# Performance work log

Hardware: AMD Instinct MI355X
Metric: run time of the kernel (lower is better)

Reference implementation:

```python
import jax, jax.numpy as jnp
import numpy as np

BN_EPS = 1e-5
L2_EPS = 1e-12


def setup_inputs() -> dict:
    key = jax.random.key(0)
    k1, k2, k3 = jax.random.split(key, 3)
    B, N, D, K, G = 32, 2048, 512, 64, 16
    init_sc = 1.0 / np.sqrt(D)
    x = jax.random.normal(k1, (B, N, D), dtype=jnp.float32)
    clusters = init_sc * jax.random.normal(k2, (D, K + G), dtype=jnp.float32)
    clusters2 = init_sc * jax.random.normal(k3, (1, D, K), dtype=jnp.float32)
    bn_gamma = jnp.ones((K + G,), dtype=jnp.float32)
    bn_beta = jnp.zeros((K + G,), dtype=jnp.float32)
    return {"x": x, "clusters": clusters, "clusters2": clusters2,
            "bn_gamma": bn_gamma, "bn_beta": bn_beta}


def reference(x, clusters, clusters2, bn_gamma, bn_beta):
    B, N, D = x.shape
    K = clusters2.shape[-1]
    xf = x.reshape(B * N, D)
    # soft cluster assignment: [B*N, K+G]
    assn = xf @ clusters
    # BatchNorm1d (training-mode batch statistics, biased variance)
    mean = jnp.mean(assn, axis=0)
    var = jnp.var(assn, axis=0)
    assn = (assn - mean) * jax.lax.rsqrt(var + BN_EPS) * bn_gamma + bn_beta
    # softmax over clusters, then drop ghost clusters
    assn = jax.nn.softmax(assn, axis=1)[:, :K].reshape(B, N, K)
    # residual aggregation
    a_sum = jnp.sum(assn, axis=1, keepdims=True)          # [B, 1, K]
    a = a_sum * clusters2                                  # [B, D, K]
    vlad = jnp.einsum("bnk,bnd->bdk", assn, x) - a         # [B, D, K]
    # intra-normalization across feature dim D
    vlad = vlad / jnp.maximum(jnp.linalg.norm(vlad, axis=1, keepdims=True), L2_EPS)
    # flatten and global L2 normalization
    vlad = vlad.reshape(B, D * K)
    vlad = vlad / jnp.maximum(jnp.linalg.norm(vlad, axis=1, keepdims=True), L2_EPS)
    return vlad
```

## Files before the change

kernel.cpp:

```cpp
#include <hip/hip_runtime.h>
#include <hip/hip_bf16.h>
#include <stdint.h>

typedef __attribute__((ext_vector_type(8))) short short8;
typedef __attribute__((ext_vector_type(4))) float f32x4;

__device__ __forceinline__ float b2f(uint16_t u) {
  union { uint32_t i; float f; } v; v.i = ((uint32_t)u) << 16; return v.f;
}
__device__ __forceinline__ uint16_t f2b(float f) {
  uint32_t u = __float_as_uint(f);
  return (uint16_t)((u + 0x7FFFu + ((u >> 16) & 1u)) >> 16);
}
__device__ __forceinline__ uint32_t pk2(uint32_t lo, uint32_t hi) {
  return __builtin_amdgcn_perm(hi + 0x8000u, lo + 0x8000u, 0x07060302u);
}

__global__ void k0_prep(const float* __restrict__ clusters,
                        uint16_t* __restrict__ cB) {
  int gid = blockIdx.x * 256 + threadIdx.x;
  if (gid < 40960) {
    int i = gid & 7, chunk = gid >> 3;
    int lr = chunk & 15, q = (chunk >> 4) & 3, c5 = chunk >> 6;
    int n = c5 % 5, kk = c5 / 5;
    cB[gid] = f2b(clusters[(kk * 32 + q * 8 + i) * 80 + n * 16 + lr]);
  }
}

__global__ __launch_bounds__(256, 4) void k1_gemm1(
    const float* __restrict__ x, const uint16_t* __restrict__ cB,
    float* __restrict__ raw, float* __restrict__ part) {
  __shared__ float sf[1280];
  const int t = threadIdx.x;
  const int w = t >> 6, lane = t & 63, q = lane >> 4, lr = lane & 15;
  const int rbase = blockIdx.x * 64 + w * 16;

  f32x4 acc[5];
#pragma unroll
  for (int n = 0; n < 5; ++n) acc[n] = 0.f;

  const float* xa = x + (size_t)(rbase + lr) * 512 + q * 8;
  const short8* cbq = (const short8*)cB + q * 16 + lr;

  uint4 u0[2], u1[2];
  u0[0] = *(const uint4*)(xa);          u1[0] = *(const uint4*)(xa + 4);
  u0[1] = *(const uint4*)(xa + 32);     u1[1] = *(const uint4*)(xa + 36);
  short8 bfc[5], bfp[5];
#pragma unroll
  for (int n = 0; n < 5; ++n) bfc[n] = cbq[n * 64];

#pragma unroll
  for (int kk = 0; kk < 16; ++kk) {
    const int si = kk & 1;
    union { short8 s; uint32_t u[4]; } av;
    av.u[0] = pk2(u0[si].x, u0[si].y); av.u[1] = pk2(u0[si].z, u0[si].w);
    av.u[2] = pk2(u1[si].x, u1[si].y); av.u[3] = pk2(u1[si].z, u1[si].w);
    if (kk < 15) {
#pragma unroll
      for (int n = 0; n < 5; ++n) bfp[n] = cbq[((kk + 1) * 5 + n) * 64];
    }
    if (kk < 14) {
      u0[si] = *(const uint4*)(xa + (kk + 2) * 32);
      u1[si] = *(const uint4*)(xa + (kk + 2) * 32 + 4);
    }
#pragma unroll
    for (int n = 0; n < 5; ++n)
      acc[n] = __builtin_amdgcn_mfma_f32_16x16x32_bf16(av.s, bfc[n], acc[n], 0, 0, 0);
#pragma unroll
    for (int n = 0; n < 5; ++n) bfc[n] = bfp[n];
  }

  float sums[5], sqs[5];
#pragma unroll
  for (int n = 0; n < 5; ++n) {
    float s = 0.f, qq = 0.f;
#pragma unroll
    for (int r = 0; r < 4; ++r) {
      float v = acc[n][r];
      s += v; qq += v * v;
      raw[(size_t)(rbase + q * 4 + r) * 80 + n * 16 + lr] = v;
    }
    s += __shfl_xor(s, 16);  s += __shfl_xor(s, 32);
    qq += __shfl_xor(qq, 16); qq += __shfl_xor(qq, 32);
    sums[n] = s; sqs[n] = qq;
  }

  if (lane < 16) {
#pragma unroll
    for (int n = 0; n < 5; ++n) {
      sf[w * 160 + n * 16 + lr] = sums[n];
      sf[640 + w * 160 + n * 16 + lr] = sqs[n];
    }
  }
  __syncthreads();
  if (t < 160) {
    float a0 = sf[t] + sf[160 + t] + sf[320 + t] + sf[480 + t];
    float b0 = sf[640 + t] + sf[800 + t] + sf[960 + t] + sf[1120 + t];
    part[(size_t)t * 1024 + blockIdx.x] = a0;
    part[(size_t)(160 + t) * 1024 + blockIdx.x] = b0;
  }
}

__global__ __launch_bounds__(64) void k2_stats(
    const float* __restrict__ part, const float* __restrict__ gamma,
    const float* __restrict__ beta, float* __restrict__ scsh) {
  int c = blockIdx.x, t = threadIdx.x;
  const float* p1 = part + (size_t)c * 1024;
  const float* p2 = part + (size_t)(160 + c) * 1024;
  float s1 = 0.f, s2 = 0.f;
#pragma unroll
  for (int p = 0; p < 1024; p += 64) { s1 += p1[p + t]; s2 += p2[p + t]; }
#pragma unroll
  for (int o = 1; o < 64; o <<= 1) { s1 += __shfl_xor(s1, o); s2 += __shfl_xor(s2, o); }
  if (t == 0) {
    float mean = s1 * (1.f / 65536.f);
    float var = s2 * (1.f / 65536.f) - mean * mean;
    float sc = rsqrtf(var + 1e-5f) * gamma[c];
    scsh[c] = sc;
    scsh[80 + c] = beta[c] - mean * sc;
  }
}

__global__ __launch_bounds__(256, 2) void k34_fused(
    const float* __restrict__ x, const float* __restrict__ raw_,
    const float* __restrict__ scsh, float* __restrict__ vpart,
    float* __restrict__ apart) {
  __shared__ __align__(16) uint16_t sx[2][256 * 40];
  __shared__ __align__(16) uint16_t sp[2][64 * 40];
  __shared__ float sc[80], sh[80];
  __shared__ float ared[4 * 64];

  const int t = threadIdx.x;
  const int b = blockIdx.x & 31;
  const int s = (blockIdx.x >> 5) & 3;
  const int dh = blockIdx.x >> 7;
  const int w = t >> 6, lane = t & 63, q = lane >> 4, lr = lane & 15;

  const int dq = t & 63, g = t >> 6;
  const int sgq = (dq + (dq >> 2)) & 3;
  const int r_ = t >> 3, cg = t & 7;
  const int kk_ = t & 63, ng = t >> 6;

  if (t < 80) sc[t] = scsh[t];
  else if (t < 160) sh[t - 80] = scsh[t];

  const float* xb = x + ((size_t)b * 2048 + (size_t)s * 512) * 512 + dh * 256;
  const float* rawb = raw_ + ((size_t)b * 2048 + (size_t)s * 512) * 80;

  f32x4 acc[4][4];
#pragma unroll
  for (int m = 0; m < 4; ++m)
#pragma unroll
    for (int j = 0; j < 4; ++j) acc[m][j] = 0.f;

  f32x4 xf4[8];
  float yf[10];
  float asum = 0.f;

#define XLOAD(c)                                                          \
  {                                                                       \
    const float* xc = xb + (size_t)((c) * 32 + g * 8) * 512 + dq * 4;     \
    _Pragma("unroll")                                                     \
    for (int jj = 0; jj < 8; ++jj)                                        \
      xf4[jj] = *(const f32x4*)(xc + (size_t)jj * 512);                   \
  }
#define RLOAD(c)                                                          \
  {                                                                       \
    const float* rc = rawb + (size_t)((c) * 32 + r_) * 80 + cg * 10;      \
    _Pragma("unroll")                                                     \
    for (int j = 0; j < 5; ++j) {                                         \
      float2 v2 = *(const float2*)(rc + j * 2);                           \
      yf[2 * j] = v2.x; yf[2 * j + 1] = v2.y;                             \
    }                                                                     \
  }
#define XSTORE(buf)                                                       \
  {                                                                       \
    _Pragma("unroll")                                                     \
    for (int e = 0; e < 4; ++e) {                                         \
      union { uint4 u; uint32_t w4[4]; } pv;                              \
      _Pragma("unroll")                                                   \
      for (int h = 0; h < 4; ++h)                                         \
        pv.w4[h] = pk2(__float_as_uint(xf4[2 * h][e]),                    \
                       __float_as_uint(xf4[2 * h + 1][e]));               \
      *(uint4*)&sx[buf][(dq * 4 + e) * 40 + ((g ^ sgq) << 3)] = pv.u;     \
    }                                                                     \
  }
#define SOFTMAX(buf)                                                      \
  {                                                                       \
    float yy[10]; float mx = -3.0e38f;                                    \
    _Pragma("unroll")                                                     \
    for (int j = 0; j < 10; ++j) {                                        \
      int cc = cg * 10 + j;                                               \
      yy[j] = yf[j] * sc[cc] + sh[cc];                                    \
      mx = fmaxf(mx, yy[j]);                                              \
    }                                                                     \
    mx = fmaxf(mx, __shfl_xor(mx, 1));                                    \
    mx = fmaxf(mx, __shfl_xor(mx, 2));                                    \
    mx = fmaxf(mx, __shfl_xor(mx, 4));                                    \
    float sum = 0.f;                                                      \
    _Pragma("unroll")                                                     \
    for (int j = 0; j < 10; ++j) { yy[j] = __expf(yy[j] - mx); sum += yy[j]; } \
    sum += __shfl_xor(sum, 1);                                            \
    sum += __shfl_xor(sum, 2);                                            \
    sum += __shfl_xor(sum, 4);                                            \
    float inv = 1.0f / sum;                                               \
    _Pragma("unroll")                                                     \
    for (int j = 0; j < 10; ++j) {                                        \
      int cc = cg * 10 + j;                                               \
      if (cc < 64) sp[buf][cc * 40 + r_] = f2b(yy[j] * inv);              \
    }                                                                     \
  }
#define GEMM(buf)                                                         \
  {                                                                       \
    const uint16_t* sxc = sx[buf];                                        \
    const uint16_t* spc = sp[buf];                                        \
    short8 bfr[4];                                                        \
    _Pragma("unroll")                                                     \
    for (int j = 0; j < 4; ++j)                                           \
      bfr[j] = *(const short8*)&spc[(j * 16 + lr) * 40 + (q << 3)];       \
    __builtin_amdgcn_s_setprio(1);                                        \
    _Pragma("unroll")                                                     \
    for (int m = 0; m < 4; ++m) {                                         \
      int row = w * 64 + m * 16 + lr;                                     \
      int swr = ((row >> 2) + (row >> 4)) & 3;                            \
      short8 af = *(const short8*)&sxc[row * 40 + ((q ^ swr) << 3)];      \
      _Pragma("unroll")                                                   \
      for (int j = 0; j < 4; ++j)                                         \
        acc[m][j] = __builtin_amdgcn_mfma_f32_16x16x32_bf16(af, bfr[j], acc[m][j], 0, 0, 0); \
    }                                                                     \
    __builtin_amdgcn_s_setprio(0);                                        \
    union { uint4 u; uint16_t us[8]; } pv;                                \
    pv.u = *(const uint4*)&spc[kk_ * 40 + (ng << 3)];                     \
    _Pragma("unroll")                                                     \
    for (int i = 0; i < 8; ++i) asum += b2f(pv.us[i]);                    \
  }

  XLOAD(0) RLOAD(0)
  __syncthreads();
  XSTORE(0) SOFTMAX(0)
  XLOAD(1) RLOAD(1)
  __syncthreads();

  for (int c = 0; c < 16; ++c) {
    const int cur = c & 1;
    if (c < 15) {
      XSTORE(cur ^ 1) SOFTMAX(cur ^ 1)
      if (c < 14) { XLOAD(c + 2) RLOAD(c + 2) }
    }
    GEMM(cur)
    __syncthreads();
  }
#undef XLOAD
#undef RLOAD
#undef XSTORE
#undef SOFTMAX
#undef GEMM

  ared[ng * 64 + kk_] = asum;
  __syncthreads();
  if (dh == 0 && t < 64) {
    float a = ared[t] + ared[64 + t] + ared[128 + t] + ared[192 + t];
    apart[((size_t)b * 4 + s) * 64 + t] = a;
  }

  float* vp = vpart + ((size_t)s * 32 + b) * 32768;
#pragma unroll
  for (int m = 0; m < 4; ++m)
#pragma unroll
    for (int j = 0; j < 4; ++j)
#pragma unroll
      for (int r2 = 0; r2 < 4; ++r2)
        vp[(size_t)(dh * 256 + w * 64 + m * 16 + q * 4 + r2) * 64 + j * 16 + lr] =
            acc[m][j][r2];
}

__global__ __launch_bounds__(256) void k5a_red(
    const float* __restrict__ vpart, const float* __restrict__ apart,
    const float* __restrict__ c2, float* __restrict__ vfull,
    float* __restrict__ csq) {
  __shared__ float las[64];
  __shared__ float sred[16 * 64];
  const int t = threadIdx.x, b = blockIdx.x >> 4, dg = blockIdx.x & 15;
  if (t < 64) {
    float a = 0.f;
#pragma unroll
    for (int s = 0; s < 4; ++s) a += apart[((size_t)b * 4 + s) * 64 + t];
    las[t] = a;
  }
  __syncthreads();
  const int di = t >> 4, kq = t & 15;
  const float4 lasv = *(const float4*)&las[kq * 4];
  float4 ssq = {0.f, 0.f, 0.f, 0.f};
#pragma unroll
  for (int jj = 0; jj < 2; ++jj) {
    int d = dg * 32 + jj * 16 + di;
    size_t i = (size_t)d * 64 + kq * 4;
    float4 cc = *(const float4*)(c2 + i);
    float4 v;
    v.x = -lasv.x * cc.x; v.y = -lasv.y * cc.y;
    v.z = -lasv.z * cc.z; v.w = -lasv.w * cc.w;
#pragma unroll
    for (int s = 0; s < 4; ++s) {
      float4 p = *(const float4*)(vpart + ((size_t)s * 32 + b) * 32768 + i);
      v.x += p.x; v.y += p.y; v.z += p.z; v.w += p.w;
    }
    *(float4*)(vfull + (size_t)b * 32768 + i) = v;
    ssq.x += v.x * v.x; ssq.y += v.y * v.y;
    ssq.z += v.z * v.z; ssq.w += v.w * v.w;
  }
  *(float4*)&sred[di * 64 + kq * 4] = ssq;
  __syncthreads();
  if (t < 64) {
    float s0 = 0.f;
#pragma unroll
    for (int di2 = 0; di2 < 16; ++di2) s0 += sred[di2 * 64 + t];
    csq[(size_t)blockIdx.x * 64 + t] = s0;
  }
}

__global__ __launch_bounds__(256) void k5c_norm(
    const float* __restrict__ csq, const float* __restrict__ vfull,
    float* __restrict__ out) {
  __shared__ float lv[64];
  __shared__ float gsv;
  const int t = threadIdx.x, b = blockIdx.x >> 4, seg = blockIdx.x & 15;
  if (t < 64) {
    float ssq = 0.f;
#pragma unroll
    for (int dg = 0; dg < 16; ++dg) ssq += csq[(size_t)(b * 16 + dg) * 64 + t];
    float iv = 1.0f / fmaxf(sqrtf(ssq), 1e-12f);
    lv[t] = iv;
    float contrib = ssq * iv * iv;
#pragma unroll
    for (int o = 1; o < 64; o <<= 1) contrib += __shfl_xor(contrib, o);
    if (t == 0) gsv = 1.0f / fmaxf(sqrtf(contrib), 1e-12f);
  }
  __syncthreads();
  const float gg = gsv;
#pragma unroll
  for (int u = 0; u < 2; ++u) {
    int i = seg * 2048 + u * 1024 + t * 4;
    int k0 = i & 63;
    float4 a = *(const float4*)(vfull + (size_t)b * 32768 + i);
    float4 o;
    o.x = a.x * lv[k0 + 0] * gg;
    o.y = a.y * lv[k0 + 1] * gg;
    o.z = a.z * lv[k0 + 2] * gg;
    o.w = a.w * lv[k0 + 3] * gg;
    *(float4*)&out[(size_t)b * 32768 + i] = o;
  }
}

extern "C" void kernel_launch(void* const* d_in, const int* in_sizes, int n_in,
                              void* d_out, int out_size, void* d_ws, size_t ws_size,
                              hipStream_t stream) {
  const float* x         = (const float*)d_in[0];
  const float* clusters  = (const float*)d_in[1];
  const float* clusters2 = (const float*)d_in[2];
  const float* gamma     = (const float*)d_in[3];
  const float* beta      = (const float*)d_in[4];
  float* out = (float*)d_out;
  char* ws = (char*)d_ws;

  uint16_t* cB = (uint16_t*)(ws + 0);
  float* part  = (float*)(ws + 81920);
  float* scsh  = (float*)(ws + 1392640);
  float* raw   = (float*)(ws + 1393280);
  float* vpart = (float*)(ws + 22364800);
  float* vfull = (float*)(ws + 39142016);
  float* apart = (float*)(ws + 43336320);
  float* csq   = (float*)(ws + 43369088);

  hipLaunchKernelGGL(k0_prep,   dim3(160),  dim3(256), 0, stream, clusters, cB);
  hipLaunchKernelGGL(k1_gemm1,  dim3(1024), dim3(256), 0, stream, x, cB, raw, part);
  hipLaunchKernelGGL(k2_stats,  dim3(80),   dim3(64),  0, stream, part, gamma, beta, scsh);
  hipLaunchKernelGGL(k34_fused, dim3(256),  dim3(256), 0, stream, x, raw, scsh, vpart, apart);
  hipLaunchKernelGGL(k5a_red,   dim3(512),  dim3(256), 0, stream, vpart, apart, clusters2, vfull, csq);
  hipLaunchKernelGGL(k5c_norm,  dim3(512),  dim3(256), 0, stream, csq, vfull, out);
}
```

Before: 245.2 us.

## Split BN-softmax out of fused GEMM2 into separate transposed-bf16 producer kernel

The fused k34 kernel computed BN+softmax per chunk, and the two d-half blocks each recomputed it. It is now split into k3_bnsoft, which computes the softmax once, writes transposed bf16 probabilities pT, and accumulates per-batch assignment sums with atomics. k4_gemm2 then loads the B fragments for its MFMA directly from global memory, prefetched one chunk ahead. This removes redundant softmax work and LDS traffic from the GEMM loop. The cost is an extra kernel launch, a pT round trip through global memory, and atomics on a_sum, which k0_prep now zeroes.

```diff
diff --git a/kernel.cpp b/kernel.cpp
--- a/kernel.cpp
+++ b/kernel.cpp
@@ -17,14 +17,17 @@
 }
 
 __global__ void k0_prep(const float* __restrict__ clusters,
-                        uint16_t* __restrict__ cB) {
+                        uint16_t* __restrict__ cB, float* __restrict__ a_sum) {
+  if (blockIdx.x >= 160) {
+    int z = (blockIdx.x - 160) * 256 + threadIdx.x;
+    if (z < 2048) a_sum[z] = 0.f;
+    return;
+  }
   int gid = blockIdx.x * 256 + threadIdx.x;
-  if (gid < 40960) {
-    int i = gid & 7, chunk = gid >> 3;
-    int lr = chunk & 15, q = (chunk >> 4) & 3, c5 = chunk >> 6;
-    int n = c5 % 5, kk = c5 / 5;
-    cB[gid] = f2b(clusters[(kk * 32 + q * 8 + i) * 80 + n * 16 + lr]);
-  }
+  int i = gid & 7, chunk = gid >> 3;
+  int lr = chunk & 15, q = (chunk >> 4) & 3, c5 = chunk >> 6;
+  int n = c5 % 5, kk = c5 / 5;
+  cB[gid] = f2b(clusters[(kk * 32 + q * 8 + i) * 80 + n * 16 + lr]);
 }
 
 __global__ __launch_bounds__(256, 4) void k1_gemm1(
@@ -121,15 +124,75 @@
   }
 }
 
-__global__ __launch_bounds__(256, 2) void k34_fused(
-    const float* __restrict__ x, const float* __restrict__ raw_,
-    const float* __restrict__ scsh, float* __restrict__ vpart,
-    float* __restrict__ apart) {
+__global__ __launch_bounds__(256) void k3_bnsoft(
+    const float* __restrict__ raw, const float* __restrict__ scsh,
+    uint16_t* __restrict__ pT, float* __restrict__ a_sum) {
+  __shared__ float sc[80], sh[80];
+  __shared__ __align__(16) uint16_t lpT[64 * 72];
+  __shared__ float apart[256];
+  const int t = threadIdx.x;
+  if (t < 80) sc[t] = scsh[t];
+  else if (t < 160) sh[t - 80] = scsh[t];
+  __syncthreads();
+
+  const int r = t >> 2, cg = t & 3;
+  const float* rp = raw + ((size_t)blockIdx.x * 64 + r) * 80;
+  const int cbase = cg * 20;
+
+  float y[20];
+#pragma unroll
+  for (int j = 0; j < 20; j += 4) {
+    float4 v = *(const float4*)(rp + cbase + j);
+    y[j] = v.x; y[j + 1] = v.y; y[j + 2] = v.z; y[j + 3] = v.w;
+  }
+  float mx = -3.0e38f;
+#pragma unroll
+  for (int j = 0; j < 20; ++j) {
+    int c = cbase + j;
+    y[j] = y[j] * sc[c] + sh[c];
+    mx = fmaxf(mx, y[j]);
+  }
+  mx = fmaxf(mx, __shfl_xor(mx, 1));
+  mx = fmaxf(mx, __shfl_xor(mx, 2));
+  float sum = 0.f;
+#pragma unroll
+  for (int j = 0; j < 20; ++j) { y[j] = __expf(y[j] - mx); sum += y[j]; }
+  sum += __shfl_xor(sum, 1);
+  sum += __shfl_xor(sum, 2);
+  float inv = 1.0f / sum;
+#pragma unroll
+  for (int j = 0; j < 20; ++j) {
+    int c = cbase + j;
+    if (c < 64) lpT[c * 72 + r] = f2b(y[j] * inv);
+  }
+  __syncthreads();
+
+  {
+    int k = t >> 2, ng = t & 3;
+    uint4 v0 = *(const uint4*)&lpT[k * 72 + ng * 16];
+    uint4 v1 = *(const uint4*)&lpT[k * 72 + ng * 16 + 8];
+    int b = blockIdx.x >> 5;
+    int n0 = (blockIdx.x & 31) * 64;
+    uint16_t* dst = pT + ((size_t)b * 64 + k) * 2048 + n0 + ng * 16;
+    *(uint4*)dst = v0;
+    *((uint4*)dst + 1) = v1;
+    const uint16_t* pv = &lpT[k * 72 + ng * 16];
+    float s = 0.f;
+#pragma unroll
+    for (int i = 0; i < 16; ++i) s += b2f(pv[i]);
+    apart[k * 4 + ng] = s;
+  }
+  __syncthreads();
+  if (t < 64) {
+    float s = apart[t * 4] + apart[t * 4 + 1] + apart[t * 4 + 2] + apart[t * 4 + 3];
+    atomicAdd(&a_sum[(blockIdx.x >> 5) * 64 + t], s);
+  }
+}
+
+__global__ __launch_bounds__(256, 2) void k4_gemm2(
+    const float* __restrict__ x, const uint16_t* __restrict__ pT,
+    float* __restrict__ vpart) {
   __shared__ __align__(16) uint16_t sx[2][256 * 40];
-  __shared__ __align__(16) uint16_t sp[2][64 * 40];
-  __shared__ float sc[80], sh[80];
-  __shared__ float ared[4 * 64];
-
   const int t = threadIdx.x;
   const int b = blockIdx.x & 31;
   const int s = (blockIdx.x >> 5) & 3;
@@ -138,14 +201,9 @@
 
   const int dq = t & 63, g = t >> 6;
   const int sgq = (dq + (dq >> 2)) & 3;
-  const int r_ = t >> 3, cg = t & 7;
-  const int kk_ = t & 63, ng = t >> 6;
-
-  if (t < 80) sc[t] = scsh[t];
-  else if (t < 160) sh[t - 80] = scsh[t];
 
   const float* xb = x + ((size_t)b * 2048 + (size_t)s * 512) * 512 + dh * 256;
-  const float* rawb = raw_ + ((size_t)b * 2048 + (size_t)s * 512) * 80;
+  const uint16_t* pb = pT + (size_t)b * 131072 + (size_t)s * 512 + (q << 3);
 
   f32x4 acc[4][4];
 #pragma unroll
@@ -154,8 +212,7 @@
     for (int j = 0; j < 4; ++j) acc[m][j] = 0.f;
 
   f32x4 xf4[8];
-  float yf[10];
-  float asum = 0.f;
+  short8 bfc[4], bfp[4];
 
 #define XLOAD(c)                                                          \
   {                                                                       \
@@ -163,15 +220,6 @@
     _Pragma("unroll")                                                     \
     for (int jj = 0; jj < 8; ++jj)                                        \
       xf4[jj] = *(const f32x4*)(xc + (size_t)jj * 512);                   \
-  }
-#define RLOAD(c)                                                          \
-  {                                                                       \
-    const float* rc = rawb + (size_t)((c) * 32 + r_) * 80 + cg * 10;      \
-    _Pragma("unroll")                                                     \
-    for (int j = 0; j < 5; ++j) {                                         \
-      float2 v2 = *(const float2*)(rc + j * 2);                           \
-      yf[2 * j] = v2.x; yf[2 * j + 1] = v2.y;                             \
-    }                                                                     \
   }
 #define XSTORE(buf)                                                       \
   {                                                                       \
@@ -185,83 +233,45 @@
       *(uint4*)&sx[buf][(dq * 4 + e) * 40 + ((g ^ sgq) << 3)] = pv.u;     \
     }                                                                     \
   }
-#define SOFTMAX(buf)                                                      \
+#define BLOAD(c, dst)                                                     \
   {                                                                       \
-    float yy[10]; float mx = -3.0e38f;                                    \
-    _Pragma("unroll")                                                     \
-    for (int j = 0; j < 10; ++j) {                                        \
-      int cc = cg * 10 + j;                                               \
-      yy[j] = yf[j] * sc[cc] + sh[cc];                                    \
-      mx = fmaxf(mx, yy[j]);                                              \
-    }                                                                     \
-    mx = fmaxf(mx, __shfl_xor(mx, 1));                                    \
-    mx = fmaxf(mx, __shfl_xor(mx, 2));                                    \
-    mx = fmaxf(mx, __shfl_xor(mx, 4));                                    \
-    float sum = 0.f;                                                      \
-    _Pragma("unroll")                                                     \
-    for (int j = 0; j < 10; ++j) { yy[j] = __expf(yy[j] - mx); sum += yy[j]; } \
-    sum += __shfl_xor(sum, 1);                                            \
-    sum += __shfl_xor(sum, 2);                                            \
-    sum += __shfl_xor(sum, 4);                                            \
-    float inv = 1.0f / sum;                                               \
-    _Pragma("unroll")                                                     \
-    for (int j = 0; j < 10; ++j) {                                        \
-      int cc = cg * 10 + j;                                               \
-      if (cc < 64) sp[buf][cc * 40 + r_] = f2b(yy[j] * inv);              \
-    }                                                                     \
-  }
-#define GEMM(buf)                                                         \
-  {                                                                       \
-    const uint16_t* sxc = sx[buf];                                        \
-    const uint16_t* spc = sp[buf];                                        \
-    short8 bfr[4];                                                        \
     _Pragma("unroll")                                                     \
     for (int j = 0; j < 4; ++j)                                           \
-      bfr[j] = *(const short8*)&spc[(j * 16 + lr) * 40 + (q << 3)];       \
-    __builtin_amdgcn_s_setprio(1);                                        \
-    _Pragma("unroll")                                                     \
-    for (int m = 0; m < 4; ++m) {                                         \
-      int row = w * 64 + m * 16 + lr;                                     \
-      int swr = ((row >> 2) + (row >> 4)) & 3;                            \
-      short8 af = *(const short8*)&sxc[row * 40 + ((q ^ swr) << 3)];      \
-      _Pragma("unroll")                                                   \
-      for (int j = 0; j < 4; ++j)                                         \
-        acc[m][j] = __builtin_amdgcn_mfma_f32_16x16x32_bf16(af, bfr[j], acc[m][j], 0, 0, 0); \
-    }                                                                     \
-    __builtin_amdgcn_s_setprio(0);                                        \
-    union { uint4 u; uint16_t us[8]; } pv;                                \
-    pv.u = *(const uint4*)&spc[kk_ * 40 + (ng << 3)];                     \
-    _Pragma("unroll")                                                     \
-    for (int i = 0; i < 8; ++i) asum += b2f(pv.us[i]);                    \
-  }
-
-  XLOAD(0) RLOAD(0)
-  __syncthreads();
-  XSTORE(0) SOFTMAX(0)
-  XLOAD(1) RLOAD(1)
+      dst[j] = *(const short8*)(pb + (size_t)(j * 16 + lr) * 2048 + (c) * 32); \
+  }
+
+  XLOAD(0)
+  BLOAD(0, bfc)
+  XSTORE(0)
+  XLOAD(1)
   __syncthreads();
 
   for (int c = 0; c < 16; ++c) {
     const int cur = c & 1;
     if (c < 15) {
-      XSTORE(cur ^ 1) SOFTMAX(cur ^ 1)
-      if (c < 14) { XLOAD(c + 2) RLOAD(c + 2) }
-    }
-    GEMM(cur)
+      XSTORE(cur ^ 1)
+      BLOAD(c + 1, bfp)
+      if (c < 14) XLOAD(c + 2)
+    }
+    const uint16_t* sxc = sx[cur];
+    __builtin_amdgcn_s_setprio(1);
+#pragma unroll
+    for (int m = 0; m < 4; ++m) {
+      int row = w * 64 + m * 16 + lr;
+      int swr = ((row >> 2) + (row >> 4)) & 3;
+      short8 af = *(const short8*)&sxc[row * 40 + ((q ^ swr) << 3)];
+#pragma unroll
+      for (int j = 0; j < 4; ++j)
+        acc[m][j] = __builtin_amdgcn_mfma_f32_16x16x32_bf16(af, bfc[j], acc[m][j], 0, 0, 0);
+    }
+    __builtin_amdgcn_s_setprio(0);
+#pragma unroll
+    for (int j = 0; j < 4; ++j) bfc[j] = bfp[j];
     __syncthreads();
   }
 #undef XLOAD
-#undef RLOAD
 #undef XSTORE
-#undef SOFTMAX
-#undef GEMM
-
-  ared[ng * 64 + kk_] = asum;
-  __syncthreads();
-  if (dh == 0 && t < 64) {
-    float a = ared[t] + ared[64 + t] + ared[128 + t] + ared[192 + t];
-    apart[((size_t)b * 4 + s) * 64 + t] = a;
-  }
+#undef BLOAD
 
   float* vp = vpart + ((size_t)s * 32 + b) * 32768;
 #pragma unroll
@@ -275,18 +285,13 @@
 }
 
 __global__ __launch_bounds__(256) void k5a_red(
-    const float* __restrict__ vpart, const float* __restrict__ apart,
+    const float* __restrict__ vpart, const float* __restrict__ a_sum,
     const float* __restrict__ c2, float* __restrict__ vfull,
     float* __restrict__ csq) {
   __shared__ float las[64];
   __shared__ float sred[16 * 64];
   const int t = threadIdx.x, b = blockIdx.x >> 4, dg = blockIdx.x & 15;
-  if (t < 64) {
-    float a = 0.f;
-#pragma unroll
-    for (int s = 0; s < 4; ++s) a += apart[((size_t)b * 4 + s) * 64 + t];
-    las[t] = a;
-  }
+  if (t < 64) las[t] = a_sum[b * 64 + t];
   __syncthreads();
   const int di = t >> 4, kq = t & 15;
   const float4 lasv = *(const float4*)&las[kq * 4];
@@ -365,16 +370,18 @@
   uint16_t* cB = (uint16_t*)(ws + 0);
   float* part  = (float*)(ws + 81920);
   float* scsh  = (float*)(ws + 1392640);
-  float* raw   = (float*)(ws + 1393280);
-  float* vpart = (float*)(ws + 22364800);
-  float* vfull = (float*)(ws + 39142016);
-  float* apart = (float*)(ws + 43336320);
-  float* csq   = (float*)(ws + 43369088);
-
-  hipLaunchKernelGGL(k0_prep,   dim3(160),  dim3(256), 0, stream, clusters, cB);
+  float* a_sum = (float*)(ws + 1393280);
+  float* raw   = (float*)(ws + 1401472);
+  uint16_t* pT = (uint16_t*)(ws + 22372992);
+  float* vpart = (float*)(ws + 30761600);
+  float* vfull = (float*)(ws + 47538816);
+  float* csq   = (float*)(ws + 51733120);
+
+  hipLaunchKernelGGL(k0_prep,   dim3(168),  dim3(256), 0, stream, clusters, cB, a_sum);
   hipLaunchKernelGGL(k1_gemm1,  dim3(1024), dim3(256), 0, stream, x, cB, raw, part);
   hipLaunchKernelGGL(k2_stats,  dim3(80),   dim3(64),  0, stream, part, gamma, beta, scsh);
-  hipLaunchKernelGGL(k34_fused, dim3(256),  dim3(256), 0, stream, x, raw, scsh, vpart, apart);
-  hipLaunchKernelGGL(k5a_red,   dim3(512),  dim3(256), 0, stream, vpart, apart, clusters2, vfull, csq);
+  hipLaunchKernelGGL(k3_bnsoft, dim3(1024), dim3(256), 0, stream, raw, scsh, pT, a_sum);
+  hipLaunchKernelGGL(k4_gemm2,  dim3(256),  dim3(256), 0, stream, x, pT, vpart);
+  hipLaunchKernelGGL(k5a_red,   dim3(512),  dim3(256), 0, stream, vpart, a_sum, clusters2, vfull, csq);
   hipLaunchKernelGGL(k5c_norm,  dim3(512),  dim3(256), 0, stream, csq, vfull, out);
 }
```

After: 247.9 us. Within noise of the previous version (+1.1%).
